# Kernel tuning notes

Hardware: AMD Instinct MI355X
Metric: run time of the kernel (lower is better)

Reference implementation:

```python
import jax, jax.numpy as jnp
import numpy as np

N, D_IN, N_CTRS, D_OUT = 65536, 64, 1024, 256


def setup_inputs() -> dict:
    key = jax.random.key(0)
    k_x, k_c, k_v = jax.random.split(key, 3)
    x = jax.random.normal(k_x, (N, D_IN), dtype=jnp.float32)
    # learned params: centers (init_ctrs 'random' draws from data scale), values (normal), scales s=ones
    ctrs = jax.random.normal(k_c, (N_CTRS, D_IN), dtype=jnp.float32)
    values = jax.random.normal(k_v, (N_CTRS, D_OUT), dtype=jnp.float32) * 1e-2
    s = jnp.ones((D_IN,), dtype=jnp.float32)
    return {"x": x, "ctrs": ctrs, "values": values, "s": s}


def reference(x, ctrs, values, s):
    # dist_sq[n,k] = sum_d (x[n,d]-ctrs[k,d])^2 * s[d]
    # expanded to avoid the (N, n_ctrs, d_in) broadcast intermediate:
    x_sq = jnp.einsum('nd,d->n', x * x, s)            # (N,)
    c_sq = jnp.einsum('kd,d->k', ctrs * ctrs, s)      # (K,)
    cross = jnp.einsum('nd,kd->nk', x * s, ctrs)      # (N, K)
    dist_sq = x_sq[:, None] + c_sq[None, :] - 2.0 * cross
    assignments = jax.nn.softmax(-dist_sq, axis=1)    # (N, K)
    return assignments @ values                        # (N, d_out)
```

## Files before the change

### kernel.cpp

```cpp
#include <hip/hip_runtime.h>

typedef _Float16 half_t;
typedef half_t f16x8 __attribute__((ext_vector_type(8)));
typedef float f32x4 __attribute__((ext_vector_type(4)));
typedef unsigned int u32x2 __attribute__((ext_vector_type(2)));

#define LOG2E 1.44269504088896340736f

#define NROWS 65536
#define DIN   64
#define NCTRS 1024
#define DOUT  256

#define CSWZ_OFF 0
#define CSWZ_BYTES (128 * 1024)
#define VSWZ_OFF (CSWZ_OFF + CSWZ_BYTES)
#define VSWZ_BYTES (512 * 1024)
#define CSQ_OFF  (VSWZ_OFF + VSWZ_BYTES)

#define CT_STRIDE 68

#define RESCALE_THR 8.0f

__global__ __launch_bounds__(256) void precompute_kernel(
    const float* __restrict__ ctrs, const float* __restrict__ values,
    const float* __restrict__ s, char* __restrict__ ws) {
  half_t* Cswz = (half_t*)(ws + CSWZ_OFF);
  half_t* Vswz = (half_t*)(ws + VSWZ_OFF);
  float* csq2 = (float*)(ws + CSQ_OFF);

  __shared__ half_t Vt[32 * 36];
  __shared__ half_t Ct[32 * CT_STRIDE];

  const int bid = blockIdx.x, tid = threadIdx.x;
  const int c = bid & 31, part = bid >> 5;
  const int w = tid >> 6, l = tid & 63, l4 = l >> 4, lm = l & 15;

  {
    int r = tid >> 3, f4 = tid & 7;
    float4 v = ((const float4*)values)[(size_t)(c * 32 + r) * 64 + part * 8 + f4];
    half_t* d = Vt + r * 36 + f4 * 4;
    d[0] = (half_t)v.x; d[1] = (half_t)v.y;
    d[2] = (half_t)v.z; d[3] = (half_t)v.w;
  }
  if (part == 0) {
#pragma unroll
    for (int i = 0; i < 2; ++i) {
      int idx = i * 256 + tid;
      int r = idx >> 4, c4 = (idx & 15) * 4;
      float4 v = ((const float4*)ctrs)[(size_t)(c * 32 + r) * 16 + (idx & 15)];
      Ct[r * CT_STRIDE + c4 + 0] = (half_t)v.x;
      Ct[r * CT_STRIDE + c4 + 1] = (half_t)v.y;
      Ct[r * CT_STRIDE + c4 + 2] = (half_t)v.z;
      Ct[r * CT_STRIDE + c4 + 3] = (half_t)v.w;
    }
    {
      int k = tid >> 3, dg = (tid & 7) * 8;
      const float* cp = ctrs + (size_t)(c * 32 + k) * DIN + dg;
      float acc = 0.0f;
#pragma unroll
      for (int j = 0; j < 8; ++j) acc = fmaf(cp[j] * cp[j], s[dg + j], acc);
      acc += __shfl_xor(acc, 1);
      acc += __shfl_xor(acc, 2);
      acc += __shfl_xor(acc, 4);
      if ((tid & 7) == 0) csq2[c * 32 + k] = acc * LOG2E;
    }
  }
  __syncthreads();

  if (w < 2) {
    int sl = part * 2 + w;
    f16x8 v;
#pragma unroll
    for (int j = 0; j < 8; ++j) v[j] = Vt[(l4 * 8 + j) * 36 + w * 16 + lm];
    *(f16x8*)(Vswz + ((c * 16 + sl) * 64 + l) * 8) = v;
  }
  if (part == 0) {
    int ct = w >> 1, kt = w & 1;
    f16x8 v;
#pragma unroll
    for (int j = 0; j < 8; ++j)
      v[j] = Ct[(ct * 16 + lm) * CT_STRIDE + kt * 32 + l4 * 8 + j];
    *(f16x8*)(Cswz + ((c * 4 + w) * 64 + l) * 8) = v;
  }
}

__global__ __launch_bounds__(256, 2) void attn_kernel(
    const float* __restrict__ x, const float* __restrict__ s,
    const char* __restrict__ ws, float* __restrict__ out) {
  const f16x8* __restrict__ cbase = (const f16x8*)(ws + CSWZ_OFF);
  const f16x8* __restrict__ vbase = (const f16x8*)(ws + VSWZ_OFF);
  const float* __restrict__ csq2 = (const float*)(ws + CSQ_OFF);

  const int tid = threadIdx.x;
  const int w = tid >> 6, l = tid & 63, l4 = l >> 4, lm = l & 15;
  const int rowbase = blockIdx.x * 128 + w * 32;

  f16x8 A[2][2];
#pragma unroll
  for (int rt = 0; rt < 2; ++rt) {
#pragma unroll
    for (int kt = 0; kt < 2; ++kt) {
      int din = kt * 32 + l4 * 8;
      const float* src = x + (size_t)(rowbase + rt * 16 + lm) * DIN + din;
      f16x8 a;
#pragma unroll
      for (int j = 0; j < 8; ++j) a[j] = (half_t)(src[j] * s[din + j]);
      A[rt][kt] = a;
    }
  }

  f16x8 ones;
#pragma unroll
  for (int j = 0; j < 8; ++j) ones[j] = (lm == 0) ? (half_t)1.0f : (half_t)0.0f;

  f32x4 O[2][16];
  f32x4 Lacc[2];
  float m[2] = {-1e30f, -1e30f};
#pragma unroll
  for (int rt = 0; rt < 2; ++rt) {
    Lacc[rt] = (f32x4){0.f, 0.f, 0.f, 0.f};
#pragma unroll
    for (int u = 0; u < 16; ++u) O[rt][u] = (f32x4){0.f, 0.f, 0.f, 0.f};
  }

  f16x8 nb0 = cbase[0 * 64 + l], nb1 = cbase[1 * 64 + l];
  f16x8 nb2 = cbase[2 * 64 + l], nb3 = cbase[3 * 64 + l];
  f32x4 ncs0 = *(const f32x4*)(csq2 + l4 * 4);
  f32x4 ncs1 = *(const f32x4*)(csq2 + 16 + l4 * 4);

#pragma unroll 1
  for (int c = 0; c < 32; ++c) {
    f16x8 b0 = nb0, b1 = nb1, b2 = nb2, b3 = nb3;
    f32x4 cs0 = ncs0, cs1 = ncs1;
    int cn = (c < 31) ? c + 1 : 31;
    nb0 = cbase[(cn * 4 + 0) * 64 + l];
    nb1 = cbase[(cn * 4 + 1) * 64 + l];
    nb2 = cbase[(cn * 4 + 2) * 64 + l];
    nb3 = cbase[(cn * 4 + 3) * 64 + l];
    ncs0 = *(const f32x4*)(csq2 + cn * 32 + l4 * 4);
    ncs1 = *(const f32x4*)(csq2 + cn * 32 + 16 + l4 * 4);

    f32x4 t0[2], t1[2];
#pragma unroll
    for (int rt = 0; rt < 2; ++rt) {
      f32x4 a0 = {0.f, 0.f, 0.f, 0.f}, a1 = {0.f, 0.f, 0.f, 0.f};
      a0 = __builtin_amdgcn_mfma_f32_16x16x32_f16(b0, A[rt][0], a0, 0, 0, 0);
      a0 = __builtin_amdgcn_mfma_f32_16x16x32_f16(b1, A[rt][1], a0, 0, 0, 0);
      a1 = __builtin_amdgcn_mfma_f32_16x16x32_f16(b2, A[rt][0], a1, 0, 0, 0);
      a1 = __builtin_amdgcn_mfma_f32_16x16x32_f16(b3, A[rt][1], a1, 0, 0, 0);
      t0[rt] = a0;
      t1[rt] = a1;
    }

    f16x8 vf[8];
#pragma unroll
    for (int u = 0; u < 8; ++u) vf[u] = vbase[(c * 16 + u) * 64 + l];

    f16x8 pb[2];
#pragma unroll
    for (int rt = 0; rt < 2; ++rt) {
      float v0[4], v1[4];
#pragma unroll
      for (int j = 0; j < 4; ++j) {
        v0[j] = fmaf(t0[rt][j], 2.0f * LOG2E, -cs0[j]);
        v1[j] = fmaf(t1[rt][j], 2.0f * LOG2E, -cs1[j]);
      }
      float pm = fmaxf(fmaxf(fmaxf(v0[0], v0[1]), fmaxf(v0[2], v0[3])),
                       fmaxf(fmaxf(v1[0], v1[1]), fmaxf(v1[2], v1[3])));
      pm = fmaxf(pm, __shfl_xor(pm, 16));
      pm = fmaxf(pm, __shfl_xor(pm, 32));

      if (__any(pm > m[rt] + RESCALE_THR)) {
        float mn = fmaxf(m[rt], pm);
        float f = __builtin_amdgcn_exp2f(m[rt] - mn);
        m[rt] = mn;
        Lacc[rt] *= f;
#pragma unroll
        for (int u = 0; u < 16; ++u) O[rt][u] *= f;
      }

      unsigned wds[4];
#pragma unroll
      for (int h = 0; h < 2; ++h) {
        union { half_t h2[2]; unsigned u; } qa, qb;
        qa.h2[0] = (half_t)__builtin_amdgcn_exp2f(v0[2 * h] - m[rt]);
        qa.h2[1] = (half_t)__builtin_amdgcn_exp2f(v0[2 * h + 1] - m[rt]);
        qb.h2[0] = (half_t)__builtin_amdgcn_exp2f(v1[2 * h] - m[rt]);
        qb.h2[1] = (half_t)__builtin_amdgcn_exp2f(v1[2 * h + 1] - m[rt]);
        u32x2 sw1 = __builtin_amdgcn_permlane32_swap(qa.u, qb.u, false, false);
        u32x2 sw2 = __builtin_amdgcn_permlane16_swap(sw1.x, sw1.y, false, false);
        wds[h] = sw2.x;
        wds[h + 2] = sw2.y;
      }
      union { unsigned u[4]; f16x8 v; } pk;
      pk.u[0] = wds[0]; pk.u[1] = wds[1]; pk.u[2] = wds[2]; pk.u[3] = wds[3];
      pb[rt] = pk.v;
    }

    __builtin_amdgcn_s_setprio(1);
#pragma unroll
    for (int u = 0; u < 8; ++u) {
      O[0][u] = __builtin_amdgcn_mfma_f32_16x16x32_f16(vf[u], pb[0], O[0][u], 0, 0, 0);
      O[1][u] = __builtin_amdgcn_mfma_f32_16x16x32_f16(vf[u], pb[1], O[1][u], 0, 0, 0);
    }
#pragma unroll
    for (int u = 8; u < 16; ++u) {
      f16x8 vfl = vbase[(c * 16 + u) * 64 + l];
      O[0][u] = __builtin_amdgcn_mfma_f32_16x16x32_f16(vfl, pb[0], O[0][u], 0, 0, 0);
      O[1][u] = __builtin_amdgcn_mfma_f32_16x16x32_f16(vfl, pb[1], O[1][u], 0, 0, 0);
    }
    Lacc[0] = __builtin_amdgcn_mfma_f32_16x16x32_f16(ones, pb[0], Lacc[0], 0, 0, 0);
    Lacc[1] = __builtin_amdgcn_mfma_f32_16x16x32_f16(ones, pb[1], Lacc[1], 0, 0, 0);
    __builtin_amdgcn_s_setprio(0);
  }

#pragma unroll
  for (int rt = 0; rt < 2; ++rt) {
    float lv = __shfl(Lacc[rt][0], lm);
    float inv = 1.0f / fmaxf(lv, 1e-30f);
    float* po = out + (size_t)(rowbase + rt * 16 + lm) * DOUT + l4 * 4;
#pragma unroll
    for (int u = 0; u < 16; ++u) {
      f32x4 ov = O[rt][u] * inv;
      *(f32x4*)(po + u * 16) = ov;
    }
  }
}

extern "C" void kernel_launch(void* const* d_in, const int* in_sizes, int n_in,
                              void* d_out, int out_size, void* d_ws, size_t ws_size,
                              hipStream_t stream) {
  const float* x = (const float*)d_in[0];
  const float* ctrs = (const float*)d_in[1];
  const float* values = (const float*)d_in[2];
  const float* s = (const float*)d_in[3];
  float* out = (float*)d_out;
  char* ws = (char*)d_ws;

  hipLaunchKernelGGL(precompute_kernel, dim3(256), dim3(256), 0, stream,
                     ctrs, values, s, ws);
  hipLaunchKernelGGL(attn_kernel, dim3(512), dim3(256), 0, stream,
                     x, s, ws, out);
}
```

Baseline: 156.6 us.

## Use two-pass softmax: compute exact row max first, drop online rescaling

```diff
diff --git a/kernel.cpp b/kernel.cpp
--- a/kernel.cpp
+++ b/kernel.cpp
@@ -19,8 +19,6 @@
 #define CSQ_OFF  (VSWZ_OFF + VSWZ_BYTES)
 
 #define CT_STRIDE 68
-
-#define RESCALE_THR 8.0f
 
 __global__ __launch_bounds__(256) void precompute_kernel(
     const float* __restrict__ ctrs, const float* __restrict__ values,
@@ -93,7 +91,7 @@
   const float* __restrict__ csq2 = (const float*)(ws + CSQ_OFF);
 
   const int tid = threadIdx.x;
-  const int w = tid >> 6, l = tid & 63, l4 = l >> 4, lm = l & 15;
+  const int l = tid & 63, w = tid >> 6, l4 = l >> 4, lm = l & 15;
   const int rowbase = blockIdx.x * 128 + w * 32;
 
   f16x8 A[2][2];
@@ -114,9 +112,50 @@
 #pragma unroll
   for (int j = 0; j < 8; ++j) ones[j] = (lm == 0) ? (half_t)1.0f : (half_t)0.0f;
 
+  float mreg[2] = {-1e30f, -1e30f};
+  {
+    f16x8 nb0 = cbase[0 * 64 + l], nb1 = cbase[1 * 64 + l];
+    f16x8 nb2 = cbase[2 * 64 + l], nb3 = cbase[3 * 64 + l];
+    f32x4 ncs0 = *(const f32x4*)(csq2 + l4 * 4);
+    f32x4 ncs1 = *(const f32x4*)(csq2 + 16 + l4 * 4);
+
+    for (int c = 0; c < 32; ++c) {
+      f16x8 b0 = nb0, b1 = nb1, b2 = nb2, b3 = nb3;
+      f32x4 cs0 = ncs0, cs1 = ncs1;
+      int cn = (c < 31) ? c + 1 : 31;
+      nb0 = cbase[(cn * 4 + 0) * 64 + l];
+      nb1 = cbase[(cn * 4 + 1) * 64 + l];
+      nb2 = cbase[(cn * 4 + 2) * 64 + l];
+      nb3 = cbase[(cn * 4 + 3) * 64 + l];
+      ncs0 = *(const f32x4*)(csq2 + cn * 32 + l4 * 4);
+      ncs1 = *(const f32x4*)(csq2 + cn * 32 + 16 + l4 * 4);
+#pragma unroll
+      for (int rt = 0; rt < 2; ++rt) {
+        f32x4 t0 = {0.f, 0.f, 0.f, 0.f}, t1 = {0.f, 0.f, 0.f, 0.f};
+        t0 = __builtin_amdgcn_mfma_f32_16x16x32_f16(b0, A[rt][0], t0, 0, 0, 0);
+        t0 = __builtin_amdgcn_mfma_f32_16x16x32_f16(b1, A[rt][1], t0, 0, 0, 0);
+        t1 = __builtin_amdgcn_mfma_f32_16x16x32_f16(b2, A[rt][0], t1, 0, 0, 0);
+        t1 = __builtin_amdgcn_mfma_f32_16x16x32_f16(b3, A[rt][1], t1, 0, 0, 0);
+        float pm = mreg[rt];
+#pragma unroll
+        for (int j = 0; j < 4; ++j) {
+          pm = fmaxf(pm, fmaf(t0[j], 2.0f * LOG2E, -cs0[j]));
+          pm = fmaxf(pm, fmaf(t1[j], 2.0f * LOG2E, -cs1[j]));
+        }
+        mreg[rt] = pm;
+      }
+    }
+#pragma unroll
+    for (int rt = 0; rt < 2; ++rt) {
+      float v = mreg[rt];
+      v = fmaxf(v, __shfl_xor(v, 16));
+      v = fmaxf(v, __shfl_xor(v, 32));
+      mreg[rt] = v;
+    }
+  }
+
   f32x4 O[2][16];
   f32x4 Lacc[2];
-  float m[2] = {-1e30f, -1e30f};
 #pragma unroll
   for (int rt = 0; rt < 2; ++rt) {
     Lacc[rt] = (f32x4){0.f, 0.f, 0.f, 0.f};
@@ -124,95 +163,80 @@
     for (int u = 0; u < 16; ++u) O[rt][u] = (f32x4){0.f, 0.f, 0.f, 0.f};
   }
 
-  f16x8 nb0 = cbase[0 * 64 + l], nb1 = cbase[1 * 64 + l];
-  f16x8 nb2 = cbase[2 * 64 + l], nb3 = cbase[3 * 64 + l];
-  f32x4 ncs0 = *(const f32x4*)(csq2 + l4 * 4);
-  f32x4 ncs1 = *(const f32x4*)(csq2 + 16 + l4 * 4);
-
-#pragma unroll 1
-  for (int c = 0; c < 32; ++c) {
-    f16x8 b0 = nb0, b1 = nb1, b2 = nb2, b3 = nb3;
-    f32x4 cs0 = ncs0, cs1 = ncs1;
-    int cn = (c < 31) ? c + 1 : 31;
-    nb0 = cbase[(cn * 4 + 0) * 64 + l];
-    nb1 = cbase[(cn * 4 + 1) * 64 + l];
-    nb2 = cbase[(cn * 4 + 2) * 64 + l];
-    nb3 = cbase[(cn * 4 + 3) * 64 + l];
-    ncs0 = *(const f32x4*)(csq2 + cn * 32 + l4 * 4);
-    ncs1 = *(const f32x4*)(csq2 + cn * 32 + 16 + l4 * 4);
-
-    f32x4 t0[2], t1[2];
-#pragma unroll
-    for (int rt = 0; rt < 2; ++rt) {
-      f32x4 a0 = {0.f, 0.f, 0.f, 0.f}, a1 = {0.f, 0.f, 0.f, 0.f};
-      a0 = __builtin_amdgcn_mfma_f32_16x16x32_f16(b0, A[rt][0], a0, 0, 0, 0);
-      a0 = __builtin_amdgcn_mfma_f32_16x16x32_f16(b1, A[rt][1], a0, 0, 0, 0);
-      a1 = __builtin_amdgcn_mfma_f32_16x16x32_f16(b2, A[rt][0], a1, 0, 0, 0);
-      a1 = __builtin_amdgcn_mfma_f32_16x16x32_f16(b3, A[rt][1], a1, 0, 0, 0);
-      t0[rt] = a0;
-      t1[rt] = a1;
-    }
-
-    f16x8 vf[8];
-#pragma unroll
-    for (int u = 0; u < 8; ++u) vf[u] = vbase[(c * 16 + u) * 64 + l];
-
-    f16x8 pb[2];
-#pragma unroll
-    for (int rt = 0; rt < 2; ++rt) {
-      float v0[4], v1[4];
-#pragma unroll
-      for (int j = 0; j < 4; ++j) {
-        v0[j] = fmaf(t0[rt][j], 2.0f * LOG2E, -cs0[j]);
-        v1[j] = fmaf(t1[rt][j], 2.0f * LOG2E, -cs1[j]);
-      }
-      float pm = fmaxf(fmaxf(fmaxf(v0[0], v0[1]), fmaxf(v0[2], v0[3])),
-                       fmaxf(fmaxf(v1[0], v1[1]), fmaxf(v1[2], v1[3])));
-      pm = fmaxf(pm, __shfl_xor(pm, 16));
-      pm = fmaxf(pm, __shfl_xor(pm, 32));
-
-      if (__any(pm > m[rt] + RESCALE_THR)) {
-        float mn = fmaxf(m[rt], pm);
-        float f = __builtin_amdgcn_exp2f(m[rt] - mn);
-        m[rt] = mn;
-        Lacc[rt] *= f;
-#pragma unroll
-        for (int u = 0; u < 16; ++u) O[rt][u] *= f;
-      }
-
-      unsigned wds[4];
-#pragma unroll
-      for (int h = 0; h < 2; ++h) {
-        union { half_t h2[2]; unsigned u; } qa, qb;
-        qa.h2[0] = (half_t)__builtin_amdgcn_exp2f(v0[2 * h] - m[rt]);
-        qa.h2[1] = (half_t)__builtin_amdgcn_exp2f(v0[2 * h + 1] - m[rt]);
-        qb.h2[0] = (half_t)__builtin_amdgcn_exp2f(v1[2 * h] - m[rt]);
-        qb.h2[1] = (half_t)__builtin_amdgcn_exp2f(v1[2 * h + 1] - m[rt]);
-        u32x2 sw1 = __builtin_amdgcn_permlane32_swap(qa.u, qb.u, false, false);
-        u32x2 sw2 = __builtin_amdgcn_permlane16_swap(sw1.x, sw1.y, false, false);
-        wds[h] = sw2.x;
-        wds[h + 2] = sw2.y;
-      }
-      union { unsigned u[4]; f16x8 v; } pk;
-      pk.u[0] = wds[0]; pk.u[1] = wds[1]; pk.u[2] = wds[2]; pk.u[3] = wds[3];
-      pb[rt] = pk.v;
-    }
-
-    __builtin_amdgcn_s_setprio(1);
-#pragma unroll
-    for (int u = 0; u < 8; ++u) {
-      O[0][u] = __builtin_amdgcn_mfma_f32_16x16x32_f16(vf[u], pb[0], O[0][u], 0, 0, 0);
-      O[1][u] = __builtin_amdgcn_mfma_f32_16x16x32_f16(vf[u], pb[1], O[1][u], 0, 0, 0);
-    }
-#pragma unroll
-    for (int u = 8; u < 16; ++u) {
-      f16x8 vfl = vbase[(c * 16 + u) * 64 + l];
-      O[0][u] = __builtin_amdgcn_mfma_f32_16x16x32_f16(vfl, pb[0], O[0][u], 0, 0, 0);
-      O[1][u] = __builtin_amdgcn_mfma_f32_16x16x32_f16(vfl, pb[1], O[1][u], 0, 0, 0);
-    }
-    Lacc[0] = __builtin_amdgcn_mfma_f32_16x16x32_f16(ones, pb[0], Lacc[0], 0, 0, 0);
-    Lacc[1] = __builtin_amdgcn_mfma_f32_16x16x32_f16(ones, pb[1], Lacc[1], 0, 0, 0);
-    __builtin_amdgcn_s_setprio(0);
+  {
+    f16x8 nb0 = cbase[0 * 64 + l], nb1 = cbase[1 * 64 + l];
+    f16x8 nb2 = cbase[2 * 64 + l], nb3 = cbase[3 * 64 + l];
+    f32x4 ncs0 = *(const f32x4*)(csq2 + l4 * 4);
+    f32x4 ncs1 = *(const f32x4*)(csq2 + 16 + l4 * 4);
+
+    for (int c = 0; c < 32; ++c) {
+      f16x8 b0 = nb0, b1 = nb1, b2 = nb2, b3 = nb3;
+      f32x4 cs0 = ncs0, cs1 = ncs1;
+      int cn = (c < 31) ? c + 1 : 31;
+      nb0 = cbase[(cn * 4 + 0) * 64 + l];
+      nb1 = cbase[(cn * 4 + 1) * 64 + l];
+      nb2 = cbase[(cn * 4 + 2) * 64 + l];
+      nb3 = cbase[(cn * 4 + 3) * 64 + l];
+      ncs0 = *(const f32x4*)(csq2 + cn * 32 + l4 * 4);
+      ncs1 = *(const f32x4*)(csq2 + cn * 32 + 16 + l4 * 4);
+
+      f32x4 t0[2], t1[2];
+#pragma unroll
+      for (int rt = 0; rt < 2; ++rt) {
+        f32x4 a0 = {0.f, 0.f, 0.f, 0.f}, a1 = {0.f, 0.f, 0.f, 0.f};
+        a0 = __builtin_amdgcn_mfma_f32_16x16x32_f16(b0, A[rt][0], a0, 0, 0, 0);
+        a0 = __builtin_amdgcn_mfma_f32_16x16x32_f16(b1, A[rt][1], a0, 0, 0, 0);
+        a1 = __builtin_amdgcn_mfma_f32_16x16x32_f16(b2, A[rt][0], a1, 0, 0, 0);
+        a1 = __builtin_amdgcn_mfma_f32_16x16x32_f16(b3, A[rt][1], a1, 0, 0, 0);
+        t0[rt] = a0;
+        t1[rt] = a1;
+      }
+
+      f16x8 vf[4];
+#pragma unroll
+      for (int u = 0; u < 4; ++u) vf[u] = vbase[(c * 16 + u) * 64 + l];
+
+      f16x8 pb[2];
+#pragma unroll
+      for (int rt = 0; rt < 2; ++rt) {
+        float v0[4], v1[4];
+#pragma unroll
+        for (int j = 0; j < 4; ++j) {
+          v0[j] = fmaf(t0[rt][j], 2.0f * LOG2E, -cs0[j]) - mreg[rt];
+          v1[j] = fmaf(t1[rt][j], 2.0f * LOG2E, -cs1[j]) - mreg[rt];
+        }
+        unsigned wds[4];
+#pragma unroll
+        for (int h = 0; h < 2; ++h) {
+          union { half_t h2[2]; unsigned u; } qa, qb;
+          qa.h2[0] = (half_t)__builtin_amdgcn_exp2f(v0[2 * h]);
+          qa.h2[1] = (half_t)__builtin_amdgcn_exp2f(v0[2 * h + 1]);
+          qb.h2[0] = (half_t)__builtin_amdgcn_exp2f(v1[2 * h]);
+          qb.h2[1] = (half_t)__builtin_amdgcn_exp2f(v1[2 * h + 1]);
+          u32x2 sw1 = __builtin_amdgcn_permlane32_swap(qa.u, qb.u, false, false);
+          u32x2 sw2 = __builtin_amdgcn_permlane16_swap(sw1.x, sw1.y, false, false);
+          wds[h] = sw2.x;
+          wds[h + 2] = sw2.y;
+        }
+        union { unsigned u[4]; f16x8 v; } pk;
+        pk.u[0] = wds[0]; pk.u[1] = wds[1]; pk.u[2] = wds[2]; pk.u[3] = wds[3];
+        pb[rt] = pk.v;
+      }
+
+#pragma unroll
+      for (int u = 0; u < 4; ++u) {
+        O[0][u] = __builtin_amdgcn_mfma_f32_16x16x32_f16(vf[u], pb[0], O[0][u], 0, 0, 0);
+        O[1][u] = __builtin_amdgcn_mfma_f32_16x16x32_f16(vf[u], pb[1], O[1][u], 0, 0, 0);
+      }
+#pragma unroll
+      for (int u = 4; u < 16; ++u) {
+        f16x8 vfl = vbase[(c * 16 + u) * 64 + l];
+        O[0][u] = __builtin_amdgcn_mfma_f32_16x16x32_f16(vfl, pb[0], O[0][u], 0, 0, 0);
+        O[1][u] = __builtin_amdgcn_mfma_f32_16x16x32_f16(vfl, pb[1], O[1][u], 0, 0, 0);
+      }
+      Lacc[0] = __builtin_amdgcn_mfma_f32_16x16x32_f16(ones, pb[0], Lacc[0], 0, 0, 0);
+      Lacc[1] = __builtin_amdgcn_mfma_f32_16x16x32_f16(ones, pb[1], Lacc[1], 0, 0, 0);
+    }
   }
 
 #pragma unroll
```

Measured after the change: 176.0 us. 12.4% more time.
